# Optimization experiments

Measured on AMD Instinct MI355X. Metric: run time of the kernel, lower is better.

The kernel has to match this reference:

```python
import jax, jax.numpy as jnp
import numpy as np
import math

N_NODES, N_EDGES, NNZ, D, L = 100000, 20000, 500000, 128, 4
ALPHA, LAMDA = 0.1, 0.5


def setup_inputs() -> dict:
    key = jax.random.key(0)
    ks = jax.random.split(key, 16)
    x = jax.random.normal(ks[0], (N_NODES, D), jnp.float32)
    e = jax.random.normal(ks[1], (N_EDGES, D), jnp.float32)
    nodes = jax.random.randint(ks[2], (NNZ,), 0, N_NODES)
    edges = jnp.sort(jax.random.randint(ks[3], (NNZ,), 0, N_EDGES)).at[-1].set(N_EDGES - 1)
    hyperedge_index = jnp.stack([nodes, edges]).astype(jnp.int32)
    dist_v2e = jax.random.randint(ks[4], (NNZ,), 0, 64).astype(jnp.float32)
    deg_v2e = jax.random.randint(ks[5], (NNZ,), 0, 64).astype(jnp.float32)
    dist_e2v = jax.random.randint(ks[6], (NNZ,), 0, 64).astype(jnp.float32)
    deg_e2v = jax.random.randint(ks[7], (NNZ,), 0, 64).astype(jnp.float32)
    s = 0.05
    W0 = jax.random.normal(ks[8], (D, D), jnp.float32) * s
    b0 = jnp.zeros((D,), jnp.float32)
    Wn = jax.random.normal(ks[9], (L, D, D), jnp.float32) * s
    We = jax.random.normal(ks[10], (L, D, D), jnp.float32) * s
    attn_w = jax.random.normal(ks[11], (L, 2 * D), jnp.float32) * s
    attn_b = jnp.zeros((L,), jnp.float32)
    wd_w = jax.random.normal(ks[12], (L,), jnp.float32) * s
    wd_b = jnp.zeros((L,), jnp.float32)
    wg_w = jax.random.normal(ks[13], (L,), jnp.float32) * s
    wg_b = jnp.zeros((L,), jnp.float32)
    return dict(x=x, e=e, hyperedge_index=hyperedge_index, dist_v2e=dist_v2e,
                deg_v2e=deg_v2e, dist_e2v=dist_e2v, deg_e2v=deg_e2v,
                W0=W0, b0=b0, Wn=Wn, We=We, attn_w=attn_w, attn_b=attn_b,
                wd_w=wd_w, wd_b=wd_b, wg_w=wg_w, wg_b=wg_b)


def _seg_softmax(s, idx, num):
    # numerically-stable scatter_softmax over segments idx
    m = jax.ops.segment_max(s, idx, num_segments=num)
    ex = jnp.exp(s - m[idx])
    den = jax.ops.segment_sum(ex, idx, num_segments=num)
    return ex / den[idx]


def _forward(x, e, hei, dv2e, gv2e, de2v, ge2v, W0, b0, Wn, We, aw, ab, wdw, wdb, wgw, wgb):
    nodes, edges = hei[0], hei[1]
    N, E = x.shape[0], e.shape[0]
    ones = jnp.ones(nodes.shape[0], x.dtype)
    dV = jax.ops.segment_sum(ones, nodes, num_segments=N)
    cnt = jax.ops.segment_sum(ones, edges, num_segments=E)
    dE = jax.ops.segment_sum(dV[nodes], edges, num_segments=E) / jnp.maximum(cnt, 1.0)
    degV = jnp.where(dV > 0, dV ** -0.5, 1.0)[:, None]   # [N,1]
    degE = jnp.where(dE > 0, dE ** -0.5, 1.0)[:, None]   # [E,1]

    x = jax.nn.relu(x @ W0 + b0)
    x0, e0 = x, e
    d = x.shape[1]
    for i in range(L):
        beta = math.log(LAMDA / (i + 1) + 1.0)
        # v2e attention: concat [x[nodes], e[edges]] -> softmax over edge segments
        sx1 = x @ aw[i, :d]; se1 = e @ aw[i, d:]
        s_v2e = sx1[nodes] + se1[edges] + ab[i] + dv2e * wdw[i] + wdb[i] + gv2e * wgw[i] + wgb[i]
        a_v2e = _seg_softmax(s_v2e, edges, E)[:, None]
        # e2v attention (flipped): concat [e[edges], x[nodes]] -> softmax over node segments
        se2 = e @ aw[i, :d]; sx2 = x @ aw[i, d:]
        s_e2v = se2[edges] + sx2[nodes] + ab[i] + de2v * wdw[i] + wdb[i] + ge2v * wgw[i] + wgb[i]
        a_e2v = _seg_softmax(s_e2v, nodes, N)[:, None]

        Xe1 = jax.ops.segment_sum(x[nodes] * a_v2e, edges, num_segments=E) * degE
        Xv1 = jax.ops.segment_sum(Xe1[edges] * a_e2v, nodes, num_segments=N) * degV
        Xv2 = jax.ops.segment_sum(e[edges] * a_e2v, nodes, num_segments=N) * degV
        Xe2 = jax.ops.segment_sum(Xv2[nodes] * a_v2e, edges, num_segments=E) * degE
        xm = (Xv1 + Xv2) * 0.5
        em = (Xe1 + Xe2) * 0.5
        xi = (1 - ALPHA) * xm + ALPHA * x0
        x = (1 - beta) * xi + beta * (xi @ Wn[i])
        ei = (1 - ALPHA) * em + ALPHA * e0
        e = (1 - beta) * ei + beta * (ei @ We[i])
        if i < L - 1:
            x = jax.nn.relu(x)
            e = jax.nn.relu(e)
    return x, e


def reference(x, e, hyperedge_index, dist_v2e, deg_v2e, dist_e2v, deg_e2v,
              W0, b0, Wn, We, attn_w, attn_b, wd_w, wd_b, wg_w, wg_b):
    return _forward(x, e, hyperedge_index, dist_v2e, deg_v2e, dist_e2v, deg_e2v,
                    W0, b0, Wn, We, attn_w, attn_b, wd_w, wd_b, wg_w, wg_b)
```

## Files before the change

kernel.cpp:

```cpp
#include <hip/hip_runtime.h>
#include <hip/hip_fp16.h>
#include <math.h>

#define DD 128
#define SCAN_BLOCKS 256
#define SMAX_CAP 128

typedef _Float16 f16x8 __attribute__((ext_vector_type(8)));
typedef float f32x4 __attribute__((ext_vector_type(4)));

__device__ inline float wave_sum(float v){
#pragma unroll
  for (int m = 32; m >= 1; m >>= 1) v += __shfl_xor(v, m, 64);
  return v;
}
__device__ inline int wave_sum_i(int v){
#pragma unroll
  for (int m = 32; m >= 1; m >>= 1) v += __shfl_xor(v, m, 64);
  return v;
}


__global__ void k_edge_offsets(const int* __restrict__ edges, int nnz, int E,
                               int* __restrict__ eo){
  int e = blockIdx.x * blockDim.x + threadIdx.x;
  if (e > E) return;
  int lo = 0, hi = nnz;
  while (lo < hi){ int mid = (lo + hi) >> 1; if (edges[mid] < e) lo = mid + 1; else hi = mid; }
  eo[e] = lo;
}

__global__ void k_hist(const int* __restrict__ nodes, int nnz, int* __restrict__ dV){
  int k = blockIdx.x * blockDim.x + threadIdx.x;
  if (k < nnz) atomicAdd(&dV[nodes[k]], 1);
}

__global__ __launch_bounds__(256) void k_scan_partial(const int* __restrict__ dV, int N,
                                                      int* __restrict__ part){
  int b = blockIdx.x, t = threadIdx.x;
  int chunk = (N + SCAN_BLOCKS - 1) / SCAN_BLOCKS;
  int s0 = b * chunk, s1 = min(s0 + chunk, N);
  int sum = 0;
  for (int n = s0 + t; n < s1; n += 256) sum += dV[n];
  sum = wave_sum_i(sum);
  __shared__ int wred[4];
  int lane = t & 63, wid = t >> 6;
  if (lane == 0) wred[wid] = sum;
  __syncthreads();
  if (t == 0) part[b] = wred[0] + wred[1] + wred[2] + wred[3];
}

__global__ __launch_bounds__(SCAN_BLOCKS) void k_scan_blocksums(int* __restrict__ part){
  __shared__ int sh[SCAN_BLOCKS];
  int t = threadIdx.x;
  int v = part[t];
  sh[t] = v; __syncthreads();
  for (int off = 1; off < SCAN_BLOCKS; off <<= 1){
    int add = (t >= off) ? sh[t - off] : 0;
    __syncthreads();
    sh[t] += add;
    __syncthreads();
  }
  part[t] = sh[t] - v;
}

__global__ __launch_bounds__(256) void k_scan_apply(const int* __restrict__ dV, int N, int nnz,
    const int* __restrict__ partScan, int* __restrict__ no, int* __restrict__ nfill,
    float* __restrict__ degV){
  int b = blockIdx.x, t = threadIdx.x;
  int chunk = (N + SCAN_BLOCKS - 1) / SCAN_BLOCKS;
  int s0 = b * chunk, s1 = min(s0 + chunk, N);
  int lane = t & 63, wid = t >> 6;
  __shared__ int wtot[4];
  __shared__ int s_run;
  if (t == 0) s_run = partScan[b];
  __syncthreads();
  for (int base = s0; base < s1; base += 256){
    int n = base + t;
    int d = (n < s1) ? dV[n] : 0;
    int v = d;
#pragma unroll
    for (int off = 1; off < 64; off <<= 1){
      int o = __shfl_up(v, off, 64);
      if (lane >= off) v += o;
    }
    if (lane == 63) wtot[wid] = v;
    __syncthreads();
    int run0 = s_run;
    int woff = 0;
    for (int w = 0; w < wid; w++) woff += wtot[w];
    if (n < s1){
      int excl = run0 + woff + v - d;
      no[n] = excl; nfill[n] = excl;
      degV[n] = d > 0 ? 1.0f / sqrtf((float)d) : 1.0f;
    }
    int btot = wtot[0] + wtot[1] + wtot[2] + wtot[3];
    __syncthreads();
    if (t == 0) s_run = run0 + btot;
    __syncthreads();
  }
  if (b == 0 && t == 0) no[N] = nnz;
}

__global__ void k_perm(const int* __restrict__ nodes, int nnz,
                       int* __restrict__ nfill, int* __restrict__ perm){
  int k = blockIdx.x * blockDim.x + threadIdx.x;
  if (k < nnz){ int pos = atomicAdd(&nfill[nodes[k]], 1); perm[pos] = k; }
}

__global__ void k_pack(const int* __restrict__ perm, const int* __restrict__ edges,
                       const float* __restrict__ dist, const float* __restrict__ deg,
                       int nnz, float2* __restrict__ pack){
  int j = blockIdx.x * blockDim.x + threadIdx.x;
  if (j < nnz){
    int k = perm[j];
    pack[j] = make_float2(__int_as_float(edges[k]), dist[k] + 64.f * deg[k]);
  }
}

__global__ void k_edge_deg(const int* __restrict__ nodes, const int* __restrict__ eo, int E,
                           const int* __restrict__ dV, float* __restrict__ degE){
  int e = blockIdx.x * blockDim.x + threadIdx.x;
  if (e >= E) return;
  int b = eo[e], en = eo[e + 1];
  float s = 0.f;
  for (int k = b; k < en; k++) s += (float)dV[nodes[k]];
  float cnt = (float)(en - b);
  float dE = s / fmaxf(cnt, 1.0f);
  degE[e] = dE > 0.f ? 1.0f / sqrtf(dE) : 1.0f;
}

__global__ __launch_bounds__(256) void k_einit(const float2* __restrict__ e_in2,
    const float* __restrict__ aw1, const float* __restrict__ aw2,
    int E, __half2* __restrict__ ET, __half2* __restrict__ e0h,
    float* __restrict__ se1, float* __restrict__ se2){
  int wave = threadIdx.x >> 6, lane = threadIdx.x & 63;
  int e = blockIdx.x * 4 + wave;
  if (e >= E) return;
  float2 v = e_in2[(size_t)e * 64 + lane];
  __half2 h = __floats2half2_rn(v.x, v.y);
  ET[(size_t)e * 128 + 2 * lane + 1] = h;
  e0h[(size_t)e * 64 + lane] = h;
  float2 a2v = ((const float2*)aw2)[lane];
  float2 a1v = ((const float2*)aw1)[lane];
  float s1 = v.x * a2v.x + v.y * a2v.y;
  float s2 = v.x * a1v.x + v.y * a1v.y;
  s1 = wave_sum(s1); s2 = wave_sum(s2);
  if (lane == 0){ se1[e] = s1; se2[e] = s2; }
}

__global__ void k_wcast(const float* __restrict__ W0, const float* __restrict__ Wn,
                        const float* __restrict__ We, _Float16* __restrict__ Wt){
  int idx = blockIdx.x * 256 + threadIdx.x;
  if (idx >= 9 * 16384) return;
  int m = idx >> 14, r = idx & 16383;
  int n = r >> 7, k = r & 127;
  float v;
  if (m == 0){
    v = W0[k * 128 + n];
  } else {
    int i = (m <= 4) ? m - 1 : m - 5;
    const float* src = (m <= 4) ? Wn + (size_t)i * 16384 : We + (size_t)i * 16384;
    float beta = logf(0.5f / (float)(i + 1) + 1.0f);
    v = beta * src[k * 128 + n] + ((n == k) ? (1.0f - beta) : 0.f);
  }
  Wt[(size_t)m * 16384 + n * 128 + k] = (_Float16)v;
}


__device__ inline void acc8h(const float4 q, float w, float* a){
  float2 h0 = __half22float2(*(const __half2*)&q.x);
  float2 h1 = __half22float2(*(const __half2*)&q.y);
  float2 h2v = __half22float2(*(const __half2*)&q.z);
  float2 h3 = __half22float2(*(const __half2*)&q.w);
  a[0] += w * h0.x; a[1] += w * h0.y; a[2] += w * h1.x; a[3] += w * h1.y;
  a[4] += w * h2v.x; a[5] += w * h2v.y; a[6] += w * h3.x; a[7] += w * h3.y;
}

__global__ __launch_bounds__(256) void k_sma1(
    const int* __restrict__ nodes, const int* __restrict__ eo,
    const float* __restrict__ sx1, const float* __restrict__ se1,
    const float* __restrict__ dist, const float* __restrict__ deg,
    const float* __restrict__ ab, const float* __restrict__ wdw, const float* __restrict__ wdb,
    const float* __restrict__ wgw, const float* __restrict__ wgb, int li,
    const float* __restrict__ degE, const float4* __restrict__ xh4,
    int E, float* __restrict__ a_v2e, float* __restrict__ esc, __half2* __restrict__ ET){
  __shared__ float lw[8][SMAX_CAP];
  int l32 = threadIdx.x & 31;
  int grp = threadIdx.x >> 5;
  int e = blockIdx.x * 8 + grp;
  if (e >= E) return;
  int b = eo[e], en = eo[e + 1];
  int l16 = l32 & 15, hf = l32 >> 4;
  if (b >= en){
    if (l32 == 0) esc[e] = 0.f;
    if (hf == 0){
      __half2 z = __floats2half2_rn(0.f, 0.f);
      size_t o = (size_t)e * 128 + 8 * l16;
      ET[o] = z; ET[o + 2] = z; ET[o + 4] = z; ET[o + 6] = z;
    }
    return;
  }
  float base = se1[e] + ab[li] + wdb[li] + wgb[li];
  float wd = wdw[li], wg = wgw[li];
  float m = -INFINITY;
  float sreg[4];
#pragma unroll
  for (int c = 0; c < 4; c++){
    int k = b + l32 + 32 * c;
    if (k < en){
      float s = sx1[nodes[k]] + base + dist[k] * wd + deg[k] * wg;
      sreg[c] = s; m = fmaxf(m, s);
    }
  }
  for (int k = b + l32 + SMAX_CAP; k < en; k += 32){
    float s = sx1[nodes[k]] + base + dist[k] * wd + deg[k] * wg;
    m = fmaxf(m, s);
  }
#pragma unroll
  for (int mm = 16; mm >= 1; mm >>= 1) m = fmaxf(m, __shfl_xor(m, mm, 32));
  float sum = 0.f;
#pragma unroll
  for (int c = 0; c < 4; c++){
    int k = b + l32 + 32 * c;
    if (k < en){
      float ex = __expf(sreg[c] - m);
      a_v2e[k] = ex; lw[grp][l32 + 32 * c] = ex; sum += ex;
    }
  }
  for (int k = b + l32 + SMAX_CAP; k < en; k += 32){
    float s = sx1[nodes[k]] + base + dist[k] * wd + deg[k] * wg;
    float ex = __expf(s - m);
    a_v2e[k] = ex; sum += ex;
  }
#pragma unroll
  for (int mm = 16; mm >= 1; mm >>= 1) sum += __shfl_xor(sum, mm, 32);
  float sc = degE[e] / sum;
  if (l32 == 0) esc[e] = sc;
  float a[8] = {0.f, 0.f, 0.f, 0.f, 0.f, 0.f, 0.f, 0.f};
  int k = b + hf;
  for (; k + 2 < en; k += 4){
    int n0 = nodes[k], n1 = nodes[k + 2];
    float w0 = (k - b < SMAX_CAP) ? lw[grp][k - b] : a_v2e[k];
    float w1 = (k + 2 - b < SMAX_CAP) ? lw[grp][k + 2 - b] : a_v2e[k + 2];
    float4 v0 = xh4[(size_t)n0 * 16 + l16];
    float4 v1 = xh4[(size_t)n1 * 16 + l16];
    acc8h(v0, w0, a); acc8h(v1, w1, a);
  }
  for (; k < en; k += 2){
    int n = nodes[k];
    float w = (k - b < SMAX_CAP) ? lw[grp][k - b] : a_v2e[k];
    float4 v = xh4[(size_t)n * 16 + l16];
    acc8h(v, w, a);
  }
#pragma unroll
  for (int j = 0; j < 8; j++) a[j] += __shfl_xor(a[j], 16, 32);
  if (hf == 0){
    size_t o = (size_t)e * 128 + 8 * l16;
    ET[o]     = __floats2half2_rn(a[0] * sc, a[1] * sc);
    ET[o + 2] = __floats2half2_rn(a[2] * sc, a[3] * sc);
    ET[o + 4] = __floats2half2_rn(a[4] * sc, a[5] * sc);
    ET[o + 6] = __floats2half2_rn(a[6] * sc, a[7] * sc);
  }
}

__device__ inline void acc8(const float4 q, float w, float* a1, float* a2){
  float2 x0 = __half22float2(*(const __half2*)&q.x);
  float2 e0 = __half22float2(*(const __half2*)&q.y);
  float2 x1 = __half22float2(*(const __half2*)&q.z);
  float2 e1 = __half22float2(*(const __half2*)&q.w);
  a1[0] += w * x0.x; a1[1] += w * x0.y; a1[2] += w * x1.x; a1[3] += w * x1.y;
  a2[0] += w * e0.x; a2[1] += w * e0.y; a2[2] += w * e1.x; a2[3] += w * e1.y;
}

__global__ __launch_bounds__(256) void k_agg2f(
    const float2* __restrict__ pack, const int* __restrict__ no,
    const float* __restrict__ se2, const float* __restrict__ sx2,
    const float* __restrict__ ab, const float* __restrict__ wdw, const float* __restrict__ wdb,
    const float* __restrict__ wgw, const float* __restrict__ wgb, int li,
    const float4* __restrict__ ETq,
    const float* __restrict__ degV, const __half2* __restrict__ x0h,
    int N, __half2* __restrict__ Xv2h, __half2* __restrict__ xiH){
  int l32 = threadIdx.x & 31;
  int grp = threadIdx.x >> 5;
  int n = blockIdx.x * 8 + grp;
  if (n >= N) return;
  int b = no[n], en = no[n + 1];
  float base = sx2[n] + ab[li] + wdb[li] + wgb[li];
  float wd = wdw[li], wg = wgw[li];
  float2 x0v2 = *(const float2*)&x0h[(size_t)n * 64 + 2 * l32];
  float l_run = 0.f;
  float a1[4] = {0.f, 0.f, 0.f, 0.f}, a2[4] = {0.f, 0.f, 0.f, 0.f};
  if (en - b <= 32){
    int cs = en - b;
    float s = -INFINITY; int e_l = 0;
    if (l32 < cs){
      float2 pk = pack[b + l32];
      e_l = __float_as_int(pk.x);
      int vi = (int)pk.y;
      s = se2[e_l] + base + (float)(vi & 63) * wd + (float)(vi >> 6) * wg;
    }
    float m_c = s;
#pragma unroll
    for (int mm = 16; mm >= 1; mm >>= 1) m_c = fmaxf(m_c, __shfl_xor(m_c, mm, 32));
    float p = (l32 < cs) ? __expf(s - m_c) : 0.f;
    l_run = p;
#pragma unroll
    for (int mm = 16; mm >= 1; mm >>= 1) l_run += __shfl_xor(l_run, mm, 32);
    int jj = 0;
    for (; jj + 3 < cs; jj += 4){
      float w0 = __shfl(p, jj, 32);
      float w1 = __shfl(p, jj + 1, 32);
      float w2 = __shfl(p, jj + 2, 32);
      float w3 = __shfl(p, jj + 3, 32);
      int e0i = __shfl(e_l, jj, 32);
      int e1i = __shfl(e_l, jj + 1, 32);
      int e2i = __shfl(e_l, jj + 2, 32);
      int e3i = __shfl(e_l, jj + 3, 32);
      float4 q0 = ETq[(size_t)e0i * 32 + l32];
      float4 q1 = ETq[(size_t)e1i * 32 + l32];
      float4 q2 = ETq[(size_t)e2i * 32 + l32];
      float4 q3 = ETq[(size_t)e3i * 32 + l32];
      acc8(q0, w0, a1, a2);
      acc8(q1, w1, a1, a2);
      acc8(q2, w2, a1, a2);
      acc8(q3, w3, a1, a2);
    }
    for (; jj < cs; jj++){
      float w = __shfl(p, jj, 32);
      int ei_ = __shfl(e_l, jj, 32);
      float4 q = ETq[(size_t)ei_ * 32 + l32];
      acc8(q, w, a1, a2);
    }
  } else {
    float m_run = -INFINITY;
    for (int cb = b; cb < en; cb += 32){
      int cs = min(32, en - cb);
      float s = -INFINITY; int e_l = 0;
      if (l32 < cs){
        float2 pk = pack[cb + l32];
        e_l = __float_as_int(pk.x);
        int vi = (int)pk.y;
        s = se2[e_l] + base + (float)(vi & 63) * wd + (float)(vi >> 6) * wg;
      }
      float m_c = s;
#pragma unroll
      for (int mm = 16; mm >= 1; mm >>= 1) m_c = fmaxf(m_c, __shfl_xor(m_c, mm, 32));
      float p = (l32 < cs) ? __expf(s - m_c) : 0.f;
      float l_c = p;
#pragma unroll
      for (int mm = 16; mm >= 1; mm >>= 1) l_c += __shfl_xor(l_c, mm, 32);
      float m_new = fmaxf(m_run, m_c);
      float f_old = __expf(m_run - m_new);
      float f_c = __expf(m_c - m_new);
#pragma unroll
      for (int r = 0; r < 4; r++){ a1[r] *= f_old; a2[r] *= f_old; }
      l_run = l_run * f_old + l_c * f_c;
      m_run = m_new;
      int jj = 0;
      for (; jj + 3 < cs; jj += 4){
        float w0 = __shfl(p, jj, 32) * f_c;
        float w1 = __shfl(p, jj + 1, 32) * f_c;
        float w2 = __shfl(p, jj + 2, 32) * f_c;
        float w3 = __shfl(p, jj + 3, 32) * f_c;
        int e0i = __shfl(e_l, jj, 32);
        int e1i = __shfl(e_l, jj + 1, 32);
        int e2i = __shfl(e_l, jj + 2, 32);
        int e3i = __shfl(e_l, jj + 3, 32);
        float4 q0 = ETq[(size_t)e0i * 32 + l32];
        float4 q1 = ETq[(size_t)e1i * 32 + l32];
        float4 q2 = ETq[(size_t)e2i * 32 + l32];
        float4 q3 = ETq[(size_t)e3i * 32 + l32];
        acc8(q0, w0, a1, a2);
        acc8(q1, w1, a1, a2);
        acc8(q2, w2, a1, a2);
        acc8(q3, w3, a1, a2);
      }
      for (; jj < cs; jj++){
        float w = __shfl(p, jj, 32) * f_c;
        int ei_ = __shfl(e_l, jj, 32);
        float4 q = ETq[(size_t)ei_ * 32 + l32];
        acc8(q, w, a1, a2);
      }
    }
  }
  float inv = l_run > 0.f ? 1.0f / l_run : 0.f;
  float dv = degV[n] * inv;
  float2 st;
  *(__half2*)&st.x = __floats2half2_rn(a2[0] * dv, a2[1] * dv);
  *(__half2*)&st.y = __floats2half2_rn(a2[2] * dv, a2[3] * dv);
  *(float2*)&Xv2h[(size_t)n * 64 + 2 * l32] = st;
  float2 h0 = __half22float2(*(const __half2*)&x0v2.x);
  float2 h1 = __half22float2(*(const __half2*)&x0v2.y);
  float2 xo;
  *(__half2*)&xo.x = __floats2half2_rn(0.45f * dv * (a1[0] + a2[0]) + 0.1f * h0.x,
                                       0.45f * dv * (a1[1] + a2[1]) + 0.1f * h0.y);
  *(__half2*)&xo.y = __floats2half2_rn(0.45f * dv * (a1[2] + a2[2]) + 0.1f * h1.x,
                                       0.45f * dv * (a1[3] + a2[3]) + 0.1f * h1.y);
  *(float2*)&xiH[(size_t)n * 64 + 2 * l32] = xo;
}

__global__ __launch_bounds__(256) void k_agg3(const int* __restrict__ nodes, const int* __restrict__ eo,
    const float4* __restrict__ Xv2h4, const float* __restrict__ a_v2e, const float* __restrict__ esc,
    const float4* __restrict__ ETq, const float4* __restrict__ e0h4,
    int E, __half2* __restrict__ eiH){
  int l32 = threadIdx.x & 31;
  int grp = threadIdx.x >> 5;
  int e = blockIdx.x * 8 + grp;
  if (e >= E) return;
  int b = eo[e], en = eo[e + 1];
  int l16 = l32 & 15, hf = l32 >> 4;
  float a[8] = {0.f, 0.f, 0.f, 0.f, 0.f, 0.f, 0.f, 0.f};
  int k = b + hf;
  for (; k + 2 < en; k += 4){
    int n0 = nodes[k], n1 = nodes[k + 2];
    float w0 = a_v2e[k], w1 = a_v2e[k + 2];
    float4 v0 = Xv2h4[(size_t)n0 * 16 + l16];
    float4 v1 = Xv2h4[(size_t)n1 * 16 + l16];
    acc8h(v0, w0, a); acc8h(v1, w1, a);
  }
  for (; k < en; k += 2){
    int n = nodes[k];
    float w = a_v2e[k];
    float4 v = Xv2h4[(size_t)n * 16 + l16];
    acc8h(v, w, a);
  }
#pragma unroll
  for (int j = 0; j < 8; j++) a[j] += __shfl_xor(a[j], 16, 32);
  if (hf == 0){
    float dE = esc[e];
    float4 q0 = ETq[(size_t)e * 32 + 2 * l16];
    float4 q1 = ETq[(size_t)e * 32 + 2 * l16 + 1];
    float2 x01 = __half22float2(*(const __half2*)&q0.x);
    float2 x23 = __half22float2(*(const __half2*)&q0.z);
    float2 x45 = __half22float2(*(const __half2*)&q1.x);
    float2 x67 = __half22float2(*(const __half2*)&q1.z);
    float4 ev = e0h4[(size_t)e * 16 + l16];
    float2 g0 = __half22float2(*(const __half2*)&ev.x);
    float2 g1 = __half22float2(*(const __half2*)&ev.y);
    float2 g2 = __half22float2(*(const __half2*)&ev.z);
    float2 g3 = __half22float2(*(const __half2*)&ev.w);
    float4 o;
    *(__half2*)&o.x = __floats2half2_rn(0.45f * (x01.x + a[0] * dE) + 0.1f * g0.x,
                                        0.45f * (x01.y + a[1] * dE) + 0.1f * g0.y);
    *(__half2*)&o.y = __floats2half2_rn(0.45f * (x23.x + a[2] * dE) + 0.1f * g1.x,
                                        0.45f * (x23.y + a[3] * dE) + 0.1f * g1.y);
    *(__half2*)&o.z = __floats2half2_rn(0.45f * (x45.x + a[4] * dE) + 0.1f * g2.x,
                                        0.45f * (x45.y + a[5] * dE) + 0.1f * g2.y);
    *(__half2*)&o.w = __floats2half2_rn(0.45f * (x67.x + a[6] * dE) + 0.1f * g3.x,
                                        0.45f * (x67.y + a[7] * dE) + 0.1f * g3.y);
    *(float4*)&eiH[(size_t)e * 64 + 4 * l16] = o;
  }
}

__device__ __forceinline__ void gemm_body(
    const _Float16* __restrict__ Ah, const _Float16* __restrict__ Wt,
    float* __restrict__ outf, _Float16* __restrict__ outh, int et,
    const float* __restrict__ awA, const float* __restrict__ awB,
    float* __restrict__ sA, float* __restrict__ sB,
    int nrows, int do_relu, int row0){
  int lane = threadIdx.x & 63;
  int lm = lane & 15;
  int lk8 = (lane >> 4) * 8;
  int arow = row0 + lm; if (arow >= nrows) arow = nrows - 1;
  f16x8 afrag[4];
#pragma unroll
  for (int ks = 0; ks < 4; ks++)
    afrag[ks] = *(const f16x8*)(Ah + (size_t)arow * 128 + ks * 32 + lk8);
  int rbase = (lane >> 4) * 4;
  float da[4] = {0.f, 0.f, 0.f, 0.f}, db[4] = {0.f, 0.f, 0.f, 0.f};
  for (int t = 0; t < 8; t++){
    f32x4 acc = {0.f, 0.f, 0.f, 0.f};
#pragma unroll
    for (int ks = 0; ks < 4; ks++){
      f16x8 bf = *(const f16x8*)(Wt + (size_t)(t * 16 + lm) * 128 + ks * 32 + lk8);
      acc = __builtin_amdgcn_mfma_f32_16x16x32_f16(afrag[ks], bf, acc, 0, 0, 0);
    }
    int col = t * 16 + lm;
    float wa = 0.f, wb = 0.f;
    if (awA){ wa = awA[col]; wb = awB[col]; }
#pragma unroll
    for (int r = 0; r < 4; r++){
      int gr = row0 + rbase + r;
      if (gr >= nrows) continue;
      float v = acc[r];
      if (do_relu) v = fmaxf(v, 0.f);
      if (outf) outf[(size_t)gr * 128 + col] = v;
      if (outh){
        if (et) outh[(size_t)gr * 256 + (col >> 1) * 4 + 2 + (col & 1)] = (_Float16)v;
        else    outh[(size_t)gr * 128 + col] = (_Float16)v;
      }
      da[r] += v * wa; db[r] += v * wb;
    }
  }
  if (awA){
#pragma unroll
    for (int r = 0; r < 4; r++){
      float a = da[r], bb = db[r];
#pragma unroll
      for (int m = 8; m >= 1; m >>= 1){
        a += __shfl_xor(a, m, 64);
        bb += __shfl_xor(bb, m, 64);
      }
      int gr = row0 + rbase + r;
      if (lm == 0 && gr < nrows){ sA[gr] = a; sB[gr] = bb; }
    }
  }
}

__global__ __launch_bounds__(256) void k_gemm2(
    const _Float16* __restrict__ Ax, const _Float16* __restrict__ Wx,
    const _Float16* __restrict__ Ae, const _Float16* __restrict__ Wte,
    float* __restrict__ outfx, _Float16* __restrict__ outhx,
    float* __restrict__ outfe, _Float16* __restrict__ outhe,
    const float* __restrict__ awAx, const float* __restrict__ awBx,
    float* __restrict__ sAx, float* __restrict__ sBx,
    const float* __restrict__ awAe, const float* __restrict__ awBe,
    float* __restrict__ sAe, float* __restrict__ sBe,
    int nrx, int nre, int nbx, int do_relu){
  int wave = threadIdx.x >> 6;
  if ((int)blockIdx.x < nbx){
    int row0 = blockIdx.x * 64 + wave * 16;
    if (row0 >= nrx) return;
    gemm_body(Ax, Wx, outfx, outhx, 0, awAx, awBx, sAx, sBx, nrx, do_relu, row0);
  } else {
    int row0 = (blockIdx.x - nbx) * 64 + wave * 16;
    if (row0 >= nre) return;
    gemm_body(Ae, Wte, outfe, outhe, 1, awAe, awBe, sAe, sBe, nre, do_relu, row0);
  }
}

__global__ __launch_bounds__(256) void k_gemm0(
    const float* __restrict__ Af, const _Float16* __restrict__ Wt,
    const float* __restrict__ bias,
    _Float16* __restrict__ outh, _Float16* __restrict__ outh2,
    const float* __restrict__ awA, const float* __restrict__ awB,
    float* __restrict__ sA, float* __restrict__ sB, int nrows){
  int wave = threadIdx.x >> 6, lane = threadIdx.x & 63;
  int row0 = blockIdx.x * 64 + wave * 16;
  if (row0 >= nrows) return;
  int lm = lane & 15;
  int lk8 = (lane >> 4) * 8;
  int arow = row0 + lm; if (arow >= nrows) arow = nrows - 1;
  const float* ap = Af + (size_t)arow * 128;
  f16x8 afrag[4];
#pragma unroll
  for (int ks = 0; ks < 4; ks++){
    float4 v0 = *(const float4*)(ap + ks * 32 + lk8);
    float4 v1 = *(const float4*)(ap + ks * 32 + lk8 + 4);
    f16x8 a;
    a[0] = (_Float16)v0.x; a[1] = (_Float16)v0.y; a[2] = (_Float16)v0.z; a[3] = (_Float16)v0.w;
    a[4] = (_Float16)v1.x; a[5] = (_Float16)v1.y; a[6] = (_Float16)v1.z; a[7] = (_Float16)v1.w;
    afrag[ks] = a;
  }
  int rbase = (lane >> 4) * 4;
  float da[4] = {0.f, 0.f, 0.f, 0.f}, db[4] = {0.f, 0.f, 0.f, 0.f};
  for (int t = 0; t < 8; t++){
    f32x4 acc = {0.f, 0.f, 0.f, 0.f};
#pragma unroll
    for (int ks = 0; ks < 4; ks++){
      f16x8 bf = *(const f16x8*)(Wt + (size_t)(t * 16 + lm) * 128 + ks * 32 + lk8);
      acc = __builtin_amdgcn_mfma_f32_16x16x32_f16(afrag[ks], bf, acc, 0, 0, 0);
    }
    int col = t * 16 + lm;
    float wa = awA[col], wb = awB[col];
    float bi = bias[col];
#pragma unroll
    for (int r = 0; r < 4; r++){
      int gr = row0 + rbase + r;
      if (gr >= nrows) continue;
      float v = fmaxf(acc[r] + bi, 0.f);
      outh[(size_t)gr * 128 + col] = (_Float16)v;
      outh2[(size_t)gr * 128 + col] = (_Float16)v;
      da[r] += v * wa; db[r] += v * wb;
    }
  }
#pragma unroll
  for (int r = 0; r < 4; r++){
    float a = da[r], bb = db[r];
#pragma unroll
    for (int m = 8; m >= 1; m >>= 1){
      a += __shfl_xor(a, m, 64);
      bb += __shfl_xor(bb, m, 64);
    }
    int gr = row0 + rbase + r;
    if (lm == 0 && gr < nrows){ sA[gr] = a; sB[gr] = bb; }
  }
}


extern "C" void kernel_launch(void* const* d_in, const int* in_sizes, int n_in,
                              void* d_out, int out_size, void* d_ws, size_t ws_size,
                              hipStream_t stream) {
  const float* x_in     = (const float*)d_in[0];
  const float* e_in     = (const float*)d_in[1];
  const int*   hei      = (const int*)d_in[2];
  const float* dist_v2e = (const float*)d_in[3];
  const float* deg_v2e  = (const float*)d_in[4];
  const float* dist_e2v = (const float*)d_in[5];
  const float* deg_e2v  = (const float*)d_in[6];
  const float* W0       = (const float*)d_in[7];
  const float* b0       = (const float*)d_in[8];
  const float* Wn       = (const float*)d_in[9];
  const float* We       = (const float*)d_in[10];
  const float* attn_w   = (const float*)d_in[11];
  const float* attn_b   = (const float*)d_in[12];
  const float* wd_w     = (const float*)d_in[13];
  const float* wd_b     = (const float*)d_in[14];
  const float* wg_w     = (const float*)d_in[15];
  const float* wg_b     = (const float*)d_in[16];

  const int N   = in_sizes[0] / DD;
  const int E   = in_sizes[1] / DD;
  const int NNZ = in_sizes[2] / 2;
  const int* nodesArr = hei;
  const int* edgesArr = hei + NNZ;

  float* out_x = (float*)d_out;
  float* out_e = (float*)d_out + (size_t)N * DD;

  __half2* Xv2h = (__half2*)out_x;
  __half2* xh   = (__half2*)((char*)out_x + (size_t)N * DD * 2);
  __half2* ET   = (__half2*)out_e;
  const float4* ETq = (const float4*)out_e;

  char* wsp = (char*)d_ws;
  auto alloc = [&](size_t bytes) -> void* {
    void* p = (void*)wsp;
    wsp += (bytes + 255) / 256 * 256;
    return p;
  };
  _Float16* x0h  = (_Float16*)alloc((size_t)N * DD * 2);
  _Float16* xiH  = (_Float16*)alloc((size_t)N * DD * 2);
  _Float16* eiH  = (_Float16*)alloc((size_t)E * DD * 2);
  _Float16* e0h  = (_Float16*)alloc((size_t)E * DD * 2);
  _Float16* Wt   = (_Float16*)alloc((size_t)9 * 16384 * 2);
  float* sx1   = (float*)alloc((size_t)N * 4);
  float* sx2   = (float*)alloc((size_t)N * 4);
  float* se1   = (float*)alloc((size_t)E * 4);
  float* se2   = (float*)alloc((size_t)E * 4);
  float* a_v2e = (float*)alloc((size_t)NNZ * 4);
  float* degV  = (float*)alloc((size_t)N * 4);
  float* degE  = (float*)alloc((size_t)E * 4);
  float* esc   = (float*)alloc((size_t)E * 4);
  float2* pack = (float2*)alloc((size_t)NNZ * 8);
  int* dV_i  = (int*)alloc((size_t)N * 4);
  int* no_   = (int*)alloc((size_t)(N + 1) * 4);
  int* nfill = (int*)alloc((size_t)N * 4);
  int* perm  = (int*)alloc((size_t)NNZ * 4);
  int* eo    = (int*)alloc((size_t)(E + 1) * 4);
  int* part  = (int*)alloc((size_t)SCAN_BLOCKS * 4);

  hipMemsetAsync(dV_i, 0, (size_t)N * 4, stream);
  k_edge_offsets<<<(E + 1 + 255) / 256, 256, 0, stream>>>(edgesArr, NNZ, E, eo);
  k_hist<<<(NNZ + 255) / 256, 256, 0, stream>>>(nodesArr, NNZ, dV_i);
  k_scan_partial<<<SCAN_BLOCKS, 256, 0, stream>>>(dV_i, N, part);
  k_scan_blocksums<<<1, SCAN_BLOCKS, 0, stream>>>(part);
  k_scan_apply<<<SCAN_BLOCKS, 256, 0, stream>>>(dV_i, N, NNZ, part, no_, nfill, degV);
  k_perm<<<(NNZ + 255) / 256, 256, 0, stream>>>(nodesArr, NNZ, nfill, perm);
  k_pack<<<(NNZ + 255) / 256, 256, 0, stream>>>(perm, edgesArr, dist_e2v, deg_e2v, NNZ, pack);
  k_edge_deg<<<(E + 255) / 256, 256, 0, stream>>>(nodesArr, eo, E, dV_i, degE);
  k_wcast<<<(9 * 16384 + 255) / 256, 256, 0, stream>>>(W0, Wn, We, Wt);

  const float* aw1_0 = attn_w;
  const float* aw2_0 = attn_w + 128;

  k_einit<<<(E + 3) / 4, 256, 0, stream>>>((const float2*)e_in, aw1_0, aw2_0,
                                            E, ET, (__half2*)e0h, se1, se2);

  k_gemm0<<<(N + 63) / 64, 256, 0, stream>>>(x_in, Wt, b0,
      (_Float16*)xh, x0h, aw1_0, aw2_0, sx1, sx2, N);

  const int nbx = (N + 63) / 64, nbe = (E + 63) / 64;
  for (int i = 0; i < 4; i++){
    const float* aw1n = (i < 3) ? attn_w + (size_t)(i + 1) * 256        : nullptr;
    const float* aw2n = (i < 3) ? attn_w + (size_t)(i + 1) * 256 + 128  : nullptr;

    k_sma1<<<(E + 7) / 8, 256, 0, stream>>>(nodesArr, eo, sx1, se1,
        dist_v2e, deg_v2e, attn_b, wd_w, wd_b, wg_w, wg_b, i, degE,
        (const float4*)xh, E, a_v2e, esc, ET);

    k_agg2f<<<(N + 7) / 8, 256, 0, stream>>>(pack, no_, se2, sx2,
        attn_b, wd_w, wd_b, wg_w, wg_b, i,
        ETq, degV, (const __half2*)x0h, N, Xv2h, (__half2*)xiH);
    k_agg3<<<(E + 7) / 8, 256, 0, stream>>>(nodesArr, eo, (const float4*)Xv2h,
        a_v2e, esc, ETq, (const float4*)e0h, E, (__half2*)eiH);

    k_gemm2<<<nbx + nbe, 256, 0, stream>>>(
        xiH, Wt + (size_t)(1 + i) * 16384,
        eiH, Wt + (size_t)(5 + i) * 16384,
        (i == 3) ? out_x : nullptr, (i < 3) ? (_Float16*)xh : nullptr,
        (i == 3) ? out_e : nullptr, (i < 3) ? (_Float16*)ET : nullptr,
        aw1n, aw2n, sx1, sx2,
        aw2n, aw1n, se1, se2,
        N, E, nbx, i < 3 ? 1 : 0);
  }
}
```

Baseline: 844.8 us.

## Fuse hypergraph aggregation kernels with per-layer MFMA GEMMs through LDS staging

Replaces the separate node aggregation, edge aggregation and combined GEMM kernels with two fused kernels. Each block of 64 rows first aggregates its rows into an LDS tile, then runs the 128x128 MFMA transform and the attention-score reductions directly from LDS. This removes the global write and re-read of the intermediate xi/ei half buffers and one launch per layer. In exchange each 32-lane group processes 8 rows serially and the grid is eight times smaller, which can reduce latency hiding for the irregular gathers. The Xv2 buffer moves from the output region into workspace so the final output write cannot clobber it.

After: 1.013 ms. 19.9% more time.

```diff
diff --git a/kernel.cpp b/kernel.cpp
--- a/kernel.cpp
+++ b/kernel.cpp
@@ -273,72 +273,40 @@
   a2[0] += w * e0.x; a2[1] += w * e0.y; a2[2] += w * e1.x; a2[3] += w * e1.y;
 }
 
-__global__ __launch_bounds__(256) void k_agg2f(
+__global__ __launch_bounds__(256) void k_fx(
     const float2* __restrict__ pack, const int* __restrict__ no,
     const float* __restrict__ se2, const float* __restrict__ sx2,
     const float* __restrict__ ab, const float* __restrict__ wdw, const float* __restrict__ wdb,
     const float* __restrict__ wgw, const float* __restrict__ wgb, int li,
-    const float4* __restrict__ ETq,
-    const float* __restrict__ degV, const __half2* __restrict__ x0h,
-    int N, __half2* __restrict__ Xv2h, __half2* __restrict__ xiH){
+    const float4* __restrict__ ETq, const float* __restrict__ degV,
+    const __half2* __restrict__ x0h, int N, __half2* __restrict__ Xv2h,
+    const _Float16* __restrict__ Wt,
+    float* __restrict__ outf, _Float16* __restrict__ outh,
+    const float* __restrict__ awA, const float* __restrict__ awB,
+    float* __restrict__ sA, float* __restrict__ sB, int do_relu){
+  __shared__ _Float16 lds[64][136];
   int l32 = threadIdx.x & 31;
   int grp = threadIdx.x >> 5;
-  int n = blockIdx.x * 8 + grp;
-  if (n >= N) return;
-  int b = no[n], en = no[n + 1];
-  float base = sx2[n] + ab[li] + wdb[li] + wgb[li];
+  int row0 = blockIdx.x * 64;
+  float cadd = ab[li] + wdb[li] + wgb[li];
   float wd = wdw[li], wg = wgw[li];
-  float2 x0v2 = *(const float2*)&x0h[(size_t)n * 64 + 2 * l32];
-  float l_run = 0.f;
-  float a1[4] = {0.f, 0.f, 0.f, 0.f}, a2[4] = {0.f, 0.f, 0.f, 0.f};
-  if (en - b <= 32){
-    int cs = en - b;
-    float s = -INFINITY; int e_l = 0;
-    if (l32 < cs){
-      float2 pk = pack[b + l32];
-      e_l = __float_as_int(pk.x);
-      int vi = (int)pk.y;
-      s = se2[e_l] + base + (float)(vi & 63) * wd + (float)(vi >> 6) * wg;
-    }
-    float m_c = s;
-#pragma unroll
-    for (int mm = 16; mm >= 1; mm >>= 1) m_c = fmaxf(m_c, __shfl_xor(m_c, mm, 32));
-    float p = (l32 < cs) ? __expf(s - m_c) : 0.f;
-    l_run = p;
-#pragma unroll
-    for (int mm = 16; mm >= 1; mm >>= 1) l_run += __shfl_xor(l_run, mm, 32);
-    int jj = 0;
-    for (; jj + 3 < cs; jj += 4){
-      float w0 = __shfl(p, jj, 32);
-      float w1 = __shfl(p, jj + 1, 32);
-      float w2 = __shfl(p, jj + 2, 32);
-      float w3 = __shfl(p, jj + 3, 32);
-      int e0i = __shfl(e_l, jj, 32);
-      int e1i = __shfl(e_l, jj + 1, 32);
-      int e2i = __shfl(e_l, jj + 2, 32);
-      int e3i = __shfl(e_l, jj + 3, 32);
-      float4 q0 = ETq[(size_t)e0i * 32 + l32];
-      float4 q1 = ETq[(size_t)e1i * 32 + l32];
-      float4 q2 = ETq[(size_t)e2i * 32 + l32];
-      float4 q3 = ETq[(size_t)e3i * 32 + l32];
-      acc8(q0, w0, a1, a2);
-      acc8(q1, w1, a1, a2);
-      acc8(q2, w2, a1, a2);
-      acc8(q3, w3, a1, a2);
-    }
-    for (; jj < cs; jj++){
-      float w = __shfl(p, jj, 32);
-      int ei_ = __shfl(e_l, jj, 32);
-      float4 q = ETq[(size_t)ei_ * 32 + l32];
-      acc8(q, w, a1, a2);
-    }
-  } else {
-    float m_run = -INFINITY;
-    for (int cb = b; cb < en; cb += 32){
-      int cs = min(32, en - cb);
+  for (int it = 0; it < 8; it++){
+    int lr = it * 8 + grp;
+    int n = row0 + lr;
+    if (n >= N){
+      *(float2*)&lds[lr][4 * l32] = make_float2(0.f, 0.f);
+      continue;
+    }
+    int b = no[n], en = no[n + 1];
+    float base = sx2[n] + cadd;
+    float2 x0v2 = *(const float2*)&x0h[(size_t)n * 64 + 2 * l32];
+    float l_run = 0.f;
+    float a1[4] = {0.f, 0.f, 0.f, 0.f}, a2[4] = {0.f, 0.f, 0.f, 0.f};
+    if (en - b <= 32){
+      int cs = en - b;
       float s = -INFINITY; int e_l = 0;
       if (l32 < cs){
-        float2 pk = pack[cb + l32];
+        float2 pk = pack[b + l32];
         e_l = __float_as_int(pk.x);
         int vi = (int)pk.y;
         s = se2[e_l] + base + (float)(vi & 63) * wd + (float)(vi >> 6) * wg;
@@ -347,22 +315,15 @@
 #pragma unroll
       for (int mm = 16; mm >= 1; mm >>= 1) m_c = fmaxf(m_c, __shfl_xor(m_c, mm, 32));
       float p = (l32 < cs) ? __expf(s - m_c) : 0.f;
-      float l_c = p;
-#pragma unroll
-      for (int mm = 16; mm >= 1; mm >>= 1) l_c += __shfl_xor(l_c, mm, 32);
-      float m_new = fmaxf(m_run, m_c);
-      float f_old = __expf(m_run - m_new);
-      float f_c = __expf(m_c - m_new);
-#pragma unroll
-      for (int r = 0; r < 4; r++){ a1[r] *= f_old; a2[r] *= f_old; }
-      l_run = l_run * f_old + l_c * f_c;
-      m_run = m_new;
+      l_run = p;
+#pragma unroll
+      for (int mm = 16; mm >= 1; mm >>= 1) l_run += __shfl_xor(l_run, mm, 32);
       int jj = 0;
       for (; jj + 3 < cs; jj += 4){
-        float w0 = __shfl(p, jj, 32) * f_c;
-        float w1 = __shfl(p, jj + 1, 32) * f_c;
-        float w2 = __shfl(p, jj + 2, 32) * f_c;
-        float w3 = __shfl(p, jj + 3, 32) * f_c;
+        float w0 = __shfl(p, jj, 32);
+        float w1 = __shfl(p, jj + 1, 32);
+        float w2 = __shfl(p, jj + 2, 32);
+        float w3 = __shfl(p, jj + 3, 32);
         int e0i = __shfl(e_l, jj, 32);
         int e1i = __shfl(e_l, jj + 1, 32);
         int e2i = __shfl(e_l, jj + 2, 32);
@@ -377,96 +338,86 @@
         acc8(q3, w3, a1, a2);
       }
       for (; jj < cs; jj++){
-        float w = __shfl(p, jj, 32) * f_c;
+        float w = __shfl(p, jj, 32);
         int ei_ = __shfl(e_l, jj, 32);
         float4 q = ETq[(size_t)ei_ * 32 + l32];
         acc8(q, w, a1, a2);
       }
-    }
-  }
-  float inv = l_run > 0.f ? 1.0f / l_run : 0.f;
-  float dv = degV[n] * inv;
-  float2 st;
-  *(__half2*)&st.x = __floats2half2_rn(a2[0] * dv, a2[1] * dv);
-  *(__half2*)&st.y = __floats2half2_rn(a2[2] * dv, a2[3] * dv);
-  *(float2*)&Xv2h[(size_t)n * 64 + 2 * l32] = st;
-  float2 h0 = __half22float2(*(const __half2*)&x0v2.x);
-  float2 h1 = __half22float2(*(const __half2*)&x0v2.y);
-  float2 xo;
-  *(__half2*)&xo.x = __floats2half2_rn(0.45f * dv * (a1[0] + a2[0]) + 0.1f * h0.x,
-                                       0.45f * dv * (a1[1] + a2[1]) + 0.1f * h0.y);
-  *(__half2*)&xo.y = __floats2half2_rn(0.45f * dv * (a1[2] + a2[2]) + 0.1f * h1.x,
-                                       0.45f * dv * (a1[3] + a2[3]) + 0.1f * h1.y);
-  *(float2*)&xiH[(size_t)n * 64 + 2 * l32] = xo;
-}
-
-__global__ __launch_bounds__(256) void k_agg3(const int* __restrict__ nodes, const int* __restrict__ eo,
-    const float4* __restrict__ Xv2h4, const float* __restrict__ a_v2e, const float* __restrict__ esc,
-    const float4* __restrict__ ETq, const float4* __restrict__ e0h4,
-    int E, __half2* __restrict__ eiH){
-  int l32 = threadIdx.x & 31;
-  int grp = threadIdx.x >> 5;
-  int e = blockIdx.x * 8 + grp;
-  if (e >= E) return;
-  int b = eo[e], en = eo[e + 1];
-  int l16 = l32 & 15, hf = l32 >> 4;
-  float a[8] = {0.f, 0.f, 0.f, 0.f, 0.f, 0.f, 0.f, 0.f};
-  int k = b + hf;
-  for (; k + 2 < en; k += 4){
-    int n0 = nodes[k], n1 = nodes[k + 2];
-    float w0 = a_v2e[k], w1 = a_v2e[k + 2];
-    float4 v0 = Xv2h4[(size_t)n0 * 16 + l16];
-    float4 v1 = Xv2h4[(size_t)n1 * 16 + l16];
-    acc8h(v0, w0, a); acc8h(v1, w1, a);
-  }
-  for (; k < en; k += 2){
-    int n = nodes[k];
-    float w = a_v2e[k];
-    float4 v = Xv2h4[(size_t)n * 16 + l16];
-    acc8h(v, w, a);
-  }
-#pragma unroll
-  for (int j = 0; j < 8; j++) a[j] += __shfl_xor(a[j], 16, 32);
-  if (hf == 0){
-    float dE = esc[e];
-    float4 q0 = ETq[(size_t)e * 32 + 2 * l16];
-    float4 q1 = ETq[(size_t)e * 32 + 2 * l16 + 1];
-    float2 x01 = __half22float2(*(const __half2*)&q0.x);
-    float2 x23 = __half22float2(*(const __half2*)&q0.z);
-    float2 x45 = __half22float2(*(const __half2*)&q1.x);
-    float2 x67 = __half22float2(*(const __half2*)&q1.z);
-    float4 ev = e0h4[(size_t)e * 16 + l16];
-    float2 g0 = __half22float2(*(const __half2*)&ev.x);
-    float2 g1 = __half22float2(*(const __half2*)&ev.y);
-    float2 g2 = __half22float2(*(const __half2*)&ev.z);
-    float2 g3 = __half22float2(*(const __half2*)&ev.w);
-    float4 o;
-    *(__half2*)&o.x = __floats2half2_rn(0.45f * (x01.x + a[0] * dE) + 0.1f * g0.x,
-                                        0.45f * (x01.y + a[1] * dE) + 0.1f * g0.y);
-    *(__half2*)&o.y = __floats2half2_rn(0.45f * (x23.x + a[2] * dE) + 0.1f * g1.x,
-                                        0.45f * (x23.y + a[3] * dE) + 0.1f * g1.y);
-    *(__half2*)&o.z = __floats2half2_rn(0.45f * (x45.x + a[4] * dE) + 0.1f * g2.x,
-                                        0.45f * (x45.y + a[5] * dE) + 0.1f * g2.y);
-    *(__half2*)&o.w = __floats2half2_rn(0.45f * (x67.x + a[6] * dE) + 0.1f * g3.x,
-                                        0.45f * (x67.y + a[7] * dE) + 0.1f * g3.y);
-    *(float4*)&eiH[(size_t)e * 64 + 4 * l16] = o;
-  }
-}
-
-__device__ __forceinline__ void gemm_body(
-    const _Float16* __restrict__ Ah, const _Float16* __restrict__ Wt,
-    float* __restrict__ outf, _Float16* __restrict__ outh, int et,
-    const float* __restrict__ awA, const float* __restrict__ awB,
-    float* __restrict__ sA, float* __restrict__ sB,
-    int nrows, int do_relu, int row0){
-  int lane = threadIdx.x & 63;
-  int lm = lane & 15;
-  int lk8 = (lane >> 4) * 8;
-  int arow = row0 + lm; if (arow >= nrows) arow = nrows - 1;
+    } else {
+      float m_run = -INFINITY;
+      for (int cb = b; cb < en; cb += 32){
+        int cs = min(32, en - cb);
+        float s = -INFINITY; int e_l = 0;
+        if (l32 < cs){
+          float2 pk = pack[cb + l32];
+          e_l = __float_as_int(pk.x);
+          int vi = (int)pk.y;
+          s = se2[e_l] + base + (float)(vi & 63) * wd + (float)(vi >> 6) * wg;
+        }
+        float m_c = s;
+#pragma unroll
+        for (int mm = 16; mm >= 1; mm >>= 1) m_c = fmaxf(m_c, __shfl_xor(m_c, mm, 32));
+        float p = (l32 < cs) ? __expf(s - m_c) : 0.f;
+        float l_c = p;
+#pragma unroll
+        for (int mm = 16; mm >= 1; mm >>= 1) l_c += __shfl_xor(l_c, mm, 32);
+        float m_new = fmaxf(m_run, m_c);
+        float f_old = __expf(m_run - m_new);
+        float f_c = __expf(m_c - m_new);
+#pragma unroll
+        for (int r = 0; r < 4; r++){ a1[r] *= f_old; a2[r] *= f_old; }
+        l_run = l_run * f_old + l_c * f_c;
+        m_run = m_new;
+        int jj = 0;
+        for (; jj + 3 < cs; jj += 4){
+          float w0 = __shfl(p, jj, 32) * f_c;
+          float w1 = __shfl(p, jj + 1, 32) * f_c;
+          float w2 = __shfl(p, jj + 2, 32) * f_c;
+          float w3 = __shfl(p, jj + 3, 32) * f_c;
+          int e0i = __shfl(e_l, jj, 32);
+          int e1i = __shfl(e_l, jj + 1, 32);
+          int e2i = __shfl(e_l, jj + 2, 32);
+          int e3i = __shfl(e_l, jj + 3, 32);
+          float4 q0 = ETq[(size_t)e0i * 32 + l32];
+          float4 q1 = ETq[(size_t)e1i * 32 + l32];
+          float4 q2 = ETq[(size_t)e2i * 32 + l32];
+          float4 q3 = ETq[(size_t)e3i * 32 + l32];
+          acc8(q0, w0, a1, a2);
+          acc8(q1, w1, a1, a2);
+          acc8(q2, w2, a1, a2);
+          acc8(q3, w3, a1, a2);
+        }
+        for (; jj < cs; jj++){
+          float w = __shfl(p, jj, 32) * f_c;
+          int ei_ = __shfl(e_l, jj, 32);
+          float4 q = ETq[(size_t)ei_ * 32 + l32];
+          acc8(q, w, a1, a2);
+        }
+      }
+    }
+    float inv = l_run > 0.f ? 1.0f / l_run : 0.f;
+    float dv = degV[n] * inv;
+    float2 st;
+    *(__half2*)&st.x = __floats2half2_rn(a2[0] * dv, a2[1] * dv);
+    *(__half2*)&st.y = __floats2half2_rn(a2[2] * dv, a2[3] * dv);
+    *(float2*)&Xv2h[(size_t)n * 64 + 2 * l32] = st;
+    float2 h0 = __half22float2(*(const __half2*)&x0v2.x);
+    float2 h1 = __half22float2(*(const __half2*)&x0v2.y);
+    float2 xo;
+    *(__half2*)&xo.x = __floats2half2_rn(0.45f * dv * (a1[0] + a2[0]) + 0.1f * h0.x,
+                                         0.45f * dv * (a1[1] + a2[1]) + 0.1f * h0.y);
+    *(__half2*)&xo.y = __floats2half2_rn(0.45f * dv * (a1[2] + a2[2]) + 0.1f * h1.x,
+                                         0.45f * dv * (a1[3] + a2[3]) + 0.1f * h1.y);
+    *(float2*)&lds[lr][4 * l32] = xo;
+  }
+  __syncthreads();
+  int lane = threadIdx.x & 63, wave = threadIdx.x >> 6;
+  int lm = lane & 15, lk8 = (lane >> 4) * 8;
+  int arl = wave * 16 + lm;
   f16x8 afrag[4];
 #pragma unroll
   for (int ks = 0; ks < 4; ks++)
-    afrag[ks] = *(const f16x8*)(Ah + (size_t)arow * 128 + ks * 32 + lk8);
+    afrag[ks] = *(const f16x8*)&lds[arl][ks * 32 + lk8];
   int rbase = (lane >> 4) * 4;
   float da[4] = {0.f, 0.f, 0.f, 0.f}, db[4] = {0.f, 0.f, 0.f, 0.f};
   for (int t = 0; t < 8; t++){
@@ -481,15 +432,12 @@
     if (awA){ wa = awA[col]; wb = awB[col]; }
 #pragma unroll
     for (int r = 0; r < 4; r++){
-      int gr = row0 + rbase + r;
-      if (gr >= nrows) continue;
+      int gr = row0 + wave * 16 + rbase + r;
+      if (gr >= N) continue;
       float v = acc[r];
       if (do_relu) v = fmaxf(v, 0.f);
       if (outf) outf[(size_t)gr * 128 + col] = v;
-      if (outh){
-        if (et) outh[(size_t)gr * 256 + (col >> 1) * 4 + 2 + (col & 1)] = (_Float16)v;
-        else    outh[(size_t)gr * 128 + col] = (_Float16)v;
-      }
+      if (outh) outh[(size_t)gr * 128 + col] = (_Float16)v;
       da[r] += v * wa; db[r] += v * wb;
     }
   }
@@ -502,31 +450,119 @@
         a += __shfl_xor(a, m, 64);
         bb += __shfl_xor(bb, m, 64);
       }
-      int gr = row0 + rbase + r;
-      if (lm == 0 && gr < nrows){ sA[gr] = a; sB[gr] = bb; }
-    }
-  }
-}
-
-__global__ __launch_bounds__(256) void k_gemm2(
-    const _Float16* __restrict__ Ax, const _Float16* __restrict__ Wx,
-    const _Float16* __restrict__ Ae, const _Float16* __restrict__ Wte,
-    float* __restrict__ outfx, _Float16* __restrict__ outhx,
-    float* __restrict__ outfe, _Float16* __restrict__ outhe,
-    const float* __restrict__ awAx, const float* __restrict__ awBx,
-    float* __restrict__ sAx, float* __restrict__ sBx,
-    const float* __restrict__ awAe, const float* __restrict__ awBe,
-    float* __restrict__ sAe, float* __restrict__ sBe,
-    int nrx, int nre, int nbx, int do_relu){
-  int wave = threadIdx.x >> 6;
-  if ((int)blockIdx.x < nbx){
-    int row0 = blockIdx.x * 64 + wave * 16;
-    if (row0 >= nrx) return;
-    gemm_body(Ax, Wx, outfx, outhx, 0, awAx, awBx, sAx, sBx, nrx, do_relu, row0);
-  } else {
-    int row0 = (blockIdx.x - nbx) * 64 + wave * 16;
-    if (row0 >= nre) return;
-    gemm_body(Ae, Wte, outfe, outhe, 1, awAe, awBe, sAe, sBe, nre, do_relu, row0);
+      int gr = row0 + wave * 16 + rbase + r;
+      if (lm == 0 && gr < N){ sA[gr] = a; sB[gr] = bb; }
+    }
+  }
+}
+
+__global__ __launch_bounds__(256) void k_fe(
+    const int* __restrict__ nodes, const int* __restrict__ eo,
+    const float4* __restrict__ Xv2h4, const float* __restrict__ a_v2e,
+    const float* __restrict__ esc,
+    const float4* __restrict__ ETq, const float4* __restrict__ e0h4,
+    int E, const _Float16* __restrict__ Wt,
+    float* __restrict__ outf, _Float16* __restrict__ outh,
+    const float* __restrict__ awA, const float* __restrict__ awB,
+    float* __restrict__ sA, float* __restrict__ sB, int do_relu){
+  __shared__ _Float16 lds[64][136];
+  int l32 = threadIdx.x & 31;
+  int grp = threadIdx.x >> 5;
+  int l16 = l32 & 15, hf = l32 >> 4;
+  int row0 = blockIdx.x * 64;
+  for (int it = 0; it < 8; it++){
+    int lr = it * 8 + grp;
+    int e = row0 + lr;
+    if (e >= E){
+      if (hf == 0) *(float4*)&lds[lr][8 * l16] = make_float4(0.f, 0.f, 0.f, 0.f);
+      continue;
+    }
+    int b = eo[e], en = eo[e + 1];
+    float a[8] = {0.f, 0.f, 0.f, 0.f, 0.f, 0.f, 0.f, 0.f};
+    int k = b + hf;
+    for (; k + 2 < en; k += 4){
+      int n0 = nodes[k], n1 = nodes[k + 2];
+      float w0 = a_v2e[k], w1 = a_v2e[k + 2];
+      float4 v0 = Xv2h4[(size_t)n0 * 16 + l16];
+      float4 v1 = Xv2h4[(size_t)n1 * 16 + l16];
+      acc8h(v0, w0, a); acc8h(v1, w1, a);
+    }
+    for (; k < en; k += 2){
+      int n = nodes[k];
+      float w = a_v2e[k];
+      float4 v = Xv2h4[(size_t)n * 16 + l16];
+      acc8h(v, w, a);
+    }
+#pragma unroll
+    for (int j = 0; j < 8; j++) a[j] += __shfl_xor(a[j], 16, 32);
+    if (hf == 0){
+      float dE = esc[e];
+      float4 q0 = ETq[(size_t)e * 32 + 2 * l16];
+      float4 q1 = ETq[(size_t)e * 32 + 2 * l16 + 1];
+      float2 x01 = __half22float2(*(const __half2*)&q0.x);
+      float2 x23 = __half22float2(*(const __half2*)&q0.z);
+      float2 x45 = __half22float2(*(const __half2*)&q1.x);
+      float2 x67 = __half22float2(*(const __half2*)&q1.z);
+      float4 ev = e0h4[(size_t)e * 16 + l16];
+      float2 g0 = __half22float2(*(const __half2*)&ev.x);
+      float2 g1 = __half22float2(*(const __half2*)&ev.y);
+      float2 g2 = __half22float2(*(const __half2*)&ev.z);
+      float2 g3 = __half22float2(*(const __half2*)&ev.w);
+      float4 o;
+      *(__half2*)&o.x = __floats2half2_rn(0.45f * (x01.x + a[0] * dE) + 0.1f * g0.x,
+                                          0.45f * (x01.y + a[1] * dE) + 0.1f * g0.y);
+      *(__half2*)&o.y = __floats2half2_rn(0.45f * (x23.x + a[2] * dE) + 0.1f * g1.x,
+                                          0.45f * (x23.y + a[3] * dE) + 0.1f * g1.y);
+      *(__half2*)&o.z = __floats2half2_rn(0.45f * (x45.x + a[4] * dE) + 0.1f * g2.x,
+                                          0.45f * (x45.y + a[5] * dE) + 0.1f * g2.y);
+      *(__half2*)&o.w = __floats2half2_rn(0.45f * (x67.x + a[6] * dE) + 0.1f * g3.x,
+                                          0.45f * (x67.y + a[7] * dE) + 0.1f * g3.y);
+      *(float4*)&lds[lr][8 * l16] = o;
+    }
+  }
+  __syncthreads();
+  int lane = threadIdx.x & 63, wave = threadIdx.x >> 6;
+  int lm = lane & 15, lk8 = (lane >> 4) * 8;
+  int arl = wave * 16 + lm;
+  f16x8 afrag[4];
+#pragma unroll
+  for (int ks = 0; ks < 4; ks++)
+    afrag[ks] = *(const f16x8*)&lds[arl][ks * 32 + lk8];
+  int rbase = (lane >> 4) * 4;
+  float da[4] = {0.f, 0.f, 0.f, 0.f}, db[4] = {0.f, 0.f, 0.f, 0.f};
+  for (int t = 0; t < 8; t++){
+    f32x4 acc = {0.f, 0.f, 0.f, 0.f};
+#pragma unroll
+    for (int ks = 0; ks < 4; ks++){
+      f16x8 bf = *(const f16x8*)(Wt + (size_t)(t * 16 + lm) * 128 + ks * 32 + lk8);
+      acc = __builtin_amdgcn_mfma_f32_16x16x32_f16(afrag[ks], bf, acc, 0, 0, 0);
+    }
+    int col = t * 16 + lm;
+    float wa = 0.f, wb = 0.f;
+    if (awA){ wa = awA[col]; wb = awB[col]; }
+#pragma unroll
+    for (int r = 0; r < 4; r++){
+      int gr = row0 + wave * 16 + rbase + r;
+      if (gr >= E) continue;
+      float v = acc[r];
+      if (do_relu) v = fmaxf(v, 0.f);
+      if (outf) outf[(size_t)gr * 128 + col] = v;
+      if (outh) outh[(size_t)gr * 256 + (col >> 1) * 4 + 2 + (col & 1)] = (_Float16)v;
+      da[r] += v * wa; db[r] += v * wb;
+    }
+  }
+  if (awA){
+#pragma unroll
+    for (int r = 0; r < 4; r++){
+      float a = da[r], bb = db[r];
+#pragma unroll
+      for (int m = 8; m >= 1; m >>= 1){
+        a += __shfl_xor(a, m, 64);
+        bb += __shfl_xor(bb, m, 64);
+      }
+      int gr = row0 + wave * 16 + rbase + r;
+      if (lm == 0 && gr < E){ sA[gr] = a; sB[gr] = bb; }
+    }
   }
 }
 
@@ -619,7 +655,6 @@
   float* out_x = (float*)d_out;
   float* out_e = (float*)d_out + (size_t)N * DD;
 
-  __half2* Xv2h = (__half2*)out_x;
   __half2* xh   = (__half2*)((char*)out_x + (size_t)N * DD * 2);
   __half2* ET   = (__half2*)out_e;
   const float4* ETq = (const float4*)out_e;
@@ -631,8 +666,7 @@
     return p;
   };
   _Float16* x0h  = (_Float16*)alloc((size_t)N * DD * 2);
-  _Float16* xiH  = (_Float16*)alloc((size_t)N * DD * 2);
-  _Float16* eiH  = (_Float16*)alloc((size_t)E * DD * 2);
+  _Float16* Xv2h = (_Float16*)alloc((size_t)N * DD * 2);
   _Float16* e0h  = (_Float16*)alloc((size_t)E * DD * 2);
   _Float16* Wt   = (_Float16*)alloc((size_t)9 * 16384 * 2);
   float* sx1   = (float*)alloc((size_t)N * 4);
@@ -671,7 +705,6 @@
   k_gemm0<<<(N + 63) / 64, 256, 0, stream>>>(x_in, Wt, b0,
       (_Float16*)xh, x0h, aw1_0, aw2_0, sx1, sx2, N);
 
-  const int nbx = (N + 63) / 64, nbe = (E + 63) / 64;
   for (int i = 0; i < 4; i++){
     const float* aw1n = (i < 3) ? attn_w + (size_t)(i + 1) * 256        : nullptr;
     const float* aw2n = (i < 3) ? attn_w + (size_t)(i + 1) * 256 + 128  : nullptr;
@@ -680,19 +713,17 @@
         dist_v2e, deg_v2e, attn_b, wd_w, wd_b, wg_w, wg_b, i, degE,
         (const float4*)xh, E, a_v2e, esc, ET);
 
-    k_agg2f<<<(N + 7) / 8, 256, 0, stream>>>(pack, no_, se2, sx2,
+    k_fx<<<(N + 63) / 64, 256, 0, stream>>>(pack, no_, se2, sx2,
         attn_b, wd_w, wd_b, wg_w, wg_b, i,
-        ETq, degV, (const __half2*)x0h, N, Xv2h, (__half2*)xiH);
-    k_agg3<<<(E + 7) / 8, 256, 0, stream>>>(nodesArr, eo, (const float4*)Xv2h,
-        a_v2e, esc, ETq, (const float4*)e0h, E, (__half2*)eiH);
-
-    k_gemm2<<<nbx + nbe, 256, 0, stream>>>(
-        xiH, Wt + (size_t)(1 + i) * 16384,
-        eiH, Wt + (size_t)(5 + i) * 16384,
+        ETq, degV, (const __half2*)x0h, N, (__half2*)Xv2h,
+        Wt + (size_t)(1 + i) * 16384,
         (i == 3) ? out_x : nullptr, (i < 3) ? (_Float16*)xh : nullptr,
+        aw1n, aw2n, sx1, sx2, i < 3 ? 1 : 0);
+
+    k_fe<<<(E + 63) / 64, 256, 0, stream>>>(nodesArr, eo, (const float4*)Xv2h,
+        a_v2e, esc, ETq, (const float4*)e0h, E,
+        Wt + (size_t)(5 + i) * 16384,
         (i == 3) ? out_e : nullptr, (i < 3) ? (_Float16*)ET : nullptr,
-        aw1n, aw2n, sx1, sx2,
-        aw2n, aw1n, se1, se2,
-        N, E, nbx, i < 3 ? 1 : 0);
-  }
-}
+        aw2n, aw1n, se1, se2, i < 3 ? 1 : 0);
+  }
+}
```
